# Kernel tuning notes

Measured on AMD Instinct MI355X. Metric: run time of the kernel, lower is better.

The kernel has to match this reference:

```python
import jax, jax.numpy as jnp
import numpy as np

SEQ = 4096
HIDDEN = 4096
HEAD_DIM = 1024
NUM_HEAD = HIDDEN // HEAD_DIM  # 4


def setup_inputs() -> dict:
    key = jax.random.key(0)
    ks = jax.random.split(key, 7)
    scale = 1.0 / np.sqrt(HIDDEN)  # torch Linear default-ish init scale
    h = jax.random.normal(ks[0], (SEQ, HIDDEN), dtype=jnp.float32)
    Wq = jax.random.normal(ks[1], (NUM_HEAD, HIDDEN, HEAD_DIM), dtype=jnp.float32) * scale
    bq = jax.random.normal(ks[2], (NUM_HEAD, HEAD_DIM), dtype=jnp.float32) * scale
    Wk = jax.random.normal(ks[3], (NUM_HEAD, HIDDEN, HEAD_DIM), dtype=jnp.float32) * scale
    bk = jax.random.normal(ks[4], (NUM_HEAD, HEAD_DIM), dtype=jnp.float32) * scale
    Wv = jax.random.normal(ks[5], (NUM_HEAD, HIDDEN, HEAD_DIM), dtype=jnp.float32) * scale
    bv = jax.random.normal(ks[6], (NUM_HEAD, HEAD_DIM), dtype=jnp.float32) * scale
    return {"h": h, "Wq": Wq, "bq": bq, "Wk": Wk, "bk": bk, "Wv": Wv, "bv": bv}


def reference(h, Wq, bq, Wk, bk, Wv, bv):
    # Batched per-head projections: q/k/v [H, S, E]
    q = jnp.einsum('sd,hde->hse', h, Wq) + bq[:, None, :]
    k = jnp.einsum('sd,hde->hse', h, Wk) + bk[:, None, :]
    v = jnp.einsum('sd,hde->hse', h, Wv) + bv[:, None, :]
    # Full (non-causal) attention scores [H, S, S], scaled by sqrt(head_dim)
    s = jnp.einsum('hse,hte->hst', q, k) / jnp.sqrt(jnp.asarray(HEAD_DIM, h.dtype))
    p = jax.nn.softmax(s, axis=-1)
    out = jnp.einsum('hst,hte->hse', p, v)  # [H, S, E]
    # Concatenate heads along feature dim -> [S, H*E]
    return jnp.transpose(out, (1, 0, 2)).reshape(h.shape[0], -1)
```

## Files before the change

kernel.cpp:

```cpp
#include <hip/hip_runtime.h>

#define SEQ   4096
#define HID   4096
#define EDIM  1024
#define NHEAD 4

typedef __attribute__((ext_vector_type(8))) short short8;
typedef __attribute__((ext_vector_type(16))) float f32x16;

typedef const __attribute__((address_space(1))) void* gas_ptr;
typedef __attribute__((address_space(3))) void* las_ptr;
#define GLD16(g, l) __builtin_amdgcn_global_load_lds((gas_ptr)(g), (las_ptr)(l), 16, 0, 0)

#define BARRIER() __builtin_amdgcn_s_barrier()
#define SCHED0()  __builtin_amdgcn_sched_barrier(0)
#define LGKM0()   asm volatile("s_waitcnt lgkmcnt(0)" ::: "memory")
#define VMC(N)    asm volatile("s_waitcnt vmcnt(" #N ")" ::: "memory")

__device__ __forceinline__ unsigned short f2bf(float f) {
  union { float f; unsigned u; } v; v.f = f;
  unsigned r = v.u + 0x7fffu + ((v.u >> 16) & 1u);
  return (unsigned short)(r >> 16);
}
__device__ __forceinline__ float bf2f(unsigned short u) {
  union { unsigned u; float f; } v; v.u = ((unsigned)u) << 16;
  return v.f;
}

__global__ __launch_bounds__(256) void hconv_kernel(const float* __restrict__ in,
                                                    unsigned short* __restrict__ out) {
  size_t i = ((size_t)blockIdx.x * 256 + threadIdx.x) * 8;
  const float4 a = *(const float4*)(in + i);
  const float4 b = *(const float4*)(in + i + 4);
  short8 o;
  o[0] = (short)f2bf(a.x); o[1] = (short)f2bf(a.y);
  o[2] = (short)f2bf(a.z); o[3] = (short)f2bf(a.w);
  o[4] = (short)f2bf(b.x); o[5] = (short)f2bf(b.y);
  o[6] = (short)f2bf(b.z); o[7] = (short)f2bf(b.w);
  *(short8*)(out + i) = o;
}

__global__ __launch_bounds__(256) void wconv_kernel(const float* __restrict__ Wq,
                                                    const float* __restrict__ Wk,
                                                    const float* __restrict__ Wv,
                                                    unsigned short* __restrict__ wt) {
  const int mh = blockIdx.y;
  const int mat = mh >> 2, head = mh & 3;
  const float* W = (mat == 0 ? Wq : (mat == 1 ? Wk : Wv)) + (size_t)head * HID * EDIM;
  unsigned short* out = wt + (size_t)mh * EDIM * HID;
  const int tile = blockIdx.x;
  const int td = tile >> 4;
  const int te = tile & 15;
  __shared__ float lds[64][65];
  const int tid = threadIdx.x;
  const int r = tid >> 4, c4 = (tid & 15) * 4;
#pragma unroll
  for (int it = 0; it < 4; ++it) {
    int dr = r + 16 * it;
    const float4 v = *(const float4*)&W[(size_t)(td * 64 + dr) * EDIM + te * 64 + c4];
    lds[dr][c4 + 0] = v.x; lds[dr][c4 + 1] = v.y;
    lds[dr][c4 + 2] = v.z; lds[dr][c4 + 3] = v.w;
  }
  __syncthreads();
#pragma unroll
  for (int it = 0; it < 4; ++it) {
    int er = r + 16 * it;
    ushort4 o;
    o.x = f2bf(lds[c4 + 0][er]); o.y = f2bf(lds[c4 + 1][er]);
    o.z = f2bf(lds[c4 + 2][er]); o.w = f2bf(lds[c4 + 3][er]);
    *(ushort4*)&out[(size_t)(te * 64 + er) * HID + td * 64 + c4] = o;
  }
}

template <int MODE>
__global__ __launch_bounds__(512, 2) void gemm256_kernel(
    const unsigned short* __restrict__ Aall, const unsigned short* __restrict__ Ball,
    long long aBatch, long long bBatch, int K,
    const float* __restrict__ biasAll, long long biasBatch,
    void* __restrict__ outAll, long long outBatch, int ldOut, float scale,
    int gx, int gxy) {
  extern __shared__ char smem[];

  const int nwg = (int)gridDim.x;
  const int lin = (int)blockIdx.x;
  int wg = (lin & 7) * (nwg >> 3) + (lin >> 3);
  const int z = wg / gxy; wg -= z * gxy;
  const int by = wg / gx;
  const int bx = wg - by * gx;
  const int bm = by * 256, bn = bx * 256;

  const unsigned short* A = Aall + (size_t)z * aBatch;
  const unsigned short* B = Ball + (size_t)z * bBatch;

  const int tid = threadIdx.x;
  const int lane = tid & 63, wid = tid >> 6;
  const int wr = wid >> 2, wc = wid & 3;
  const int la31 = lane & 31, lg2 = lane >> 5;

  const int srow = tid >> 3;
  const int sk = ((tid & 7) ^ ((srow ^ (srow >> 3)) & 7)) * 8;
  const unsigned short* aS00 = A + (size_t)(bm +   0 + srow) * K + sk;
  const unsigned short* aS01 = A + (size_t)(bm +  64 + srow) * K + sk;
  const unsigned short* aS10 = A + (size_t)(bm + 128 + srow) * K + sk;
  const unsigned short* aS11 = A + (size_t)(bm + 192 + srow) * K + sk;
  const unsigned short* bS00 = B + (size_t)(bn +   0 + srow) * K + sk;
  const unsigned short* bS01 = B + (size_t)(bn +  64 + srow) * K + sk;
  const unsigned short* bS10 = B + (size_t)(bn + 128 + srow) * K + sk;
  const unsigned short* bS11 = B + (size_t)(bn + 192 + srow) * K + sk;

#define STG(p0, p1, regionOff, tt)                                        \
  do {                                                                    \
    char* _d = smem + (((tt) & 1) << 16) + (regionOff) + tid * 16;        \
    GLD16((p0) + (size_t)(tt) * 64, _d);                                  \
    GLD16((p1) + (size_t)(tt) * 64, _d + 8192);                           \
  } while (0)

  int aO[4], aX[4];
#pragma unroll
  for (int m = 0; m < 4; ++m) {
    const int arow = wr * 128 + m * 32 + la31;
    aO[m] = arow * 128;
    aX[m] = (arow ^ (arow >> 3)) & 7;
  }
  int bO[2], bX[2];
#pragma unroll
  for (int n = 0; n < 2; ++n) {
    const int brow = wc * 64 + n * 32 + la31;
    bO[n] = 32768 + brow * 128;
    bX[n] = (brow ^ (brow >> 3)) & 7;
  }

  f32x16 acc[4][2];
#pragma unroll
  for (int m = 0; m < 4; ++m)
#pragma unroll
    for (int n = 0; n < 2; ++n)
#pragma unroll
      for (int r = 0; r < 16; ++r) acc[m][n][r] = 0.f;

  const int NT = K >> 6;

  STG(aS00, aS01, 0, 0);
  STG(aS10, aS11, 16384, 0);
  STG(bS00, bS01, 32768, 0);
  STG(bS10, bS11, 49152, 0);

  short8 av[2][4], bv[2][4];

  for (int t = 0; t < NT; ++t) {
    const char* base = smem + ((t & 1) << 16);

    VMC(0);
    BARRIER();
    SCHED0();

#pragma unroll
    for (int m = 0; m < 2; ++m)
#pragma unroll
      for (int ks = 0; ks < 4; ++ks)
        av[m][ks] = *(const short8*)(base + aO[m] + ((((ks << 1) + lg2) ^ aX[m]) << 4));
#pragma unroll
    for (int n = 0; n < 2; ++n)
#pragma unroll
      for (int ks = 0; ks < 4; ++ks)
        bv[n][ks] = *(const short8*)(base + bO[n] + ((((ks << 1) + lg2) ^ bX[n]) << 4));
    if (t + 1 < NT) {
      STG(aS00, aS01, 0, t + 1);
      STG(aS10, aS11, 16384, t + 1);
      STG(bS00, bS01, 32768, t + 1);
      STG(bS10, bS11, 49152, t + 1);
    }
    LGKM0();
    SCHED0();
    __builtin_amdgcn_s_setprio(1);
#pragma unroll
    for (int ks = 0; ks < 4; ++ks)
#pragma unroll
      for (int m = 0; m < 2; ++m)
#pragma unroll
        for (int n = 0; n < 2; ++n)
          acc[m][n] = __builtin_amdgcn_mfma_f32_32x32x16_bf16(av[m][ks], bv[n][ks], acc[m][n], 0, 0, 0);
    __builtin_amdgcn_s_setprio(0);

#pragma unroll
    for (int m = 0; m < 2; ++m)
#pragma unroll
      for (int ks = 0; ks < 4; ++ks)
        av[m][ks] = *(const short8*)(base + aO[m + 2] + ((((ks << 1) + lg2) ^ aX[m + 2]) << 4));
    LGKM0();
    SCHED0();
    __builtin_amdgcn_s_setprio(1);
#pragma unroll
    for (int ks = 0; ks < 4; ++ks)
#pragma unroll
      for (int m = 0; m < 2; ++m)
#pragma unroll
        for (int n = 0; n < 2; ++n)
          acc[m + 2][n] = __builtin_amdgcn_mfma_f32_32x32x16_bf16(av[m][ks], bv[n][ks], acc[m + 2][n], 0, 0, 0);
    __builtin_amdgcn_s_setprio(0);
    SCHED0();
  }
#undef STG

  float bvv[2];
  if (MODE == 0 || MODE == 1) {
    const float* bias = biasAll + (size_t)z * biasBatch;
#pragma unroll
    for (int n = 0; n < 2; ++n) bvv[n] = bias[bn + wc * 64 + n * 32 + la31];
  }
#pragma unroll
  for (int m = 0; m < 4; ++m)
#pragma unroll
    for (int n = 0; n < 2; ++n)
#pragma unroll
      for (int r = 0; r < 16; ++r) {
        const int grow = bm + wr * 128 + m * 32 + (r & 3) + 8 * (r >> 2) + 4 * lg2;
        const int gcol = bn + wc * 64 + n * 32 + la31;
        float val = acc[m][n][r];
        if (MODE == 0 || MODE == 1) val += bvv[n];
        if (MODE == 2) val *= scale;
        if (MODE == 0 || MODE == 2) {
          unsigned short* o = (unsigned short*)outAll + (size_t)z * outBatch;
          o[(size_t)grow * ldOut + gcol] = f2bf(val);
        } else if (MODE == 1) {
          unsigned short* o = (unsigned short*)outAll + (size_t)z * outBatch;
          o[(size_t)gcol * ldOut + grow] = f2bf(val);
        } else {
          float* o = (float*)outAll + (size_t)z * outBatch;
          o[(size_t)grow * ldOut + gcol] = val;
        }
      }
}

__global__ __launch_bounds__(256) void softmax_kernel(unsigned short* __restrict__ Sb) {
  const size_t row = blockIdx.x;
  unsigned short* p = Sb + row * (size_t)SEQ;
  const int tid = threadIdx.x;
  const int lane = tid & 63, wid = tid >> 6;
  float v[16];
  const short8 u0 = *(const short8*)&p[tid * 16];
  const short8 u1 = *(const short8*)&p[tid * 16 + 8];
#pragma unroll
  for (int j = 0; j < 8; ++j) v[j] = bf2f((unsigned short)u0[j]);
#pragma unroll
  for (int j = 0; j < 8; ++j) v[8 + j] = bf2f((unsigned short)u1[j]);
  float mx = v[0];
#pragma unroll
  for (int j = 1; j < 16; ++j) mx = fmaxf(mx, v[j]);
#pragma unroll
  for (int off = 32; off; off >>= 1) mx = fmaxf(mx, __shfl_xor(mx, off));
  __shared__ float red[8];
  if (lane == 0) red[wid] = mx;
  __syncthreads();
  mx = fmaxf(fmaxf(red[0], red[1]), fmaxf(red[2], red[3]));
  float s = 0.f;
#pragma unroll
  for (int j = 0; j < 16; ++j) { v[j] = __expf(v[j] - mx); s += v[j]; }
#pragma unroll
  for (int off = 32; off; off >>= 1) s += __shfl_xor(s, off);
  if (lane == 0) red[4 + wid] = s;
  __syncthreads();
  s = (red[4] + red[5]) + (red[6] + red[7]);
  const float inv = 1.0f / s;
  short8 o0, o1;
#pragma unroll
  for (int j = 0; j < 8; ++j) o0[j] = (short)f2bf(v[j] * inv);
#pragma unroll
  for (int j = 0; j < 8; ++j) o1[j] = (short)f2bf(v[8 + j] * inv);
  *(short8*)&p[tid * 16] = o0;
  *(short8*)&p[tid * 16 + 8] = o1;
}

extern "C" void kernel_launch(void* const* d_in, const int* in_sizes, int n_in,
                              void* d_out, int out_size, void* d_ws, size_t ws_size,
                              hipStream_t stream) {
  const float* h  = (const float*)d_in[0];
  const float* Wq = (const float*)d_in[1];
  const float* bq = (const float*)d_in[2];
  const float* Wk = (const float*)d_in[3];
  const float* bk = (const float*)d_in[4];
  const float* Wv = (const float*)d_in[5];
  const float* bv = (const float*)d_in[6];
  float* out = (float*)d_out;
  char* ws = (char*)d_ws;

  (void)hipFuncSetAttribute((const void*)&gemm256_kernel<0>,
                            hipFuncAttributeMaxDynamicSharedMemorySize, 131072);
  (void)hipFuncSetAttribute((const void*)&gemm256_kernel<1>,
                            hipFuncAttributeMaxDynamicSharedMemorySize, 131072);
  (void)hipFuncSetAttribute((const void*)&gemm256_kernel<2>,
                            hipFuncAttributeMaxDynamicSharedMemorySize, 131072);
  (void)hipFuncSetAttribute((const void*)&gemm256_kernel<3>,
                            hipFuncAttributeMaxDynamicSharedMemorySize, 131072);

  unsigned short* hB = (unsigned short*)ws;
  unsigned short* wt = (unsigned short*)(ws + (32ull << 20));
  unsigned short* Sb = (unsigned short*)ws;
  unsigned short* Qb = (unsigned short*)(ws + (128ull << 20));
  unsigned short* Kb = (unsigned short*)(ws + (160ull << 20));
  unsigned short* Vt = (unsigned short*)(ws + (192ull << 20));

  const long long WED = (long long)EDIM * HID;
  const long long QKB = (long long)SEQ * EDIM;
  const long long SSB = (long long)SEQ * SEQ;

  hconv_kernel<<<dim3((SEQ * (size_t)HID) / (256 * 8)), 256, 0, stream>>>(h, hB);
  wconv_kernel<<<dim3((HID / 64) * (EDIM / 64), 12), 256, 0, stream>>>(Wq, Wk, Wv, wt);

  gemm256_kernel<0><<<dim3(4 * 16 * 4), 512, 131072, stream>>>(
      hB, wt + 0 * WED, 0, WED, HID, bq, EDIM, Qb, QKB, EDIM, 1.f, 4, 64);
  gemm256_kernel<0><<<dim3(4 * 16 * 4), 512, 131072, stream>>>(
      hB, wt + 4 * WED, 0, WED, HID, bk, EDIM, Kb, QKB, EDIM, 1.f, 4, 64);
  gemm256_kernel<1><<<dim3(4 * 16 * 4), 512, 131072, stream>>>(
      hB, wt + 8 * WED, 0, WED, HID, bv, EDIM, Vt, QKB, SEQ, 1.f, 4, 64);

  gemm256_kernel<2><<<dim3(16 * 16 * 4), 512, 131072, stream>>>(
      Qb, Kb, QKB, QKB, EDIM, nullptr, 0, Sb, SSB, SEQ, 0.03125f, 16, 256);

  softmax_kernel<<<dim3(NHEAD * SEQ), 256, 0, stream>>>(Sb);

  gemm256_kernel<3><<<dim3(4 * 16 * 4), 512, 131072, stream>>>(
      Sb, Vt, SSB, QKB, SEQ, nullptr, 0, out, (long long)EDIM, NHEAD * EDIM, 1.f, 4, 64);
}
```

Baseline: 797.4 us.

## Software-pipeline GEMM main loop with register double-buffered LDS fragments

Reworks the bf16 GEMM inner loop so each 64-wide k-tile is processed as four k-slices. The LDS fragment reads for the next slice are issued into a second register set while MFMAs run on the current one, and the first slice of the next tile is prefetched after the barrier. The explicit lgkmcnt waits are dropped, and a second barrier per iteration protects the LDS buffer before it is overwritten. The aim is to hide LDS read latency behind matrix-core work, at the cost of an extra barrier per k-tile and more scheduling pressure on the compiler.

```diff
diff --git a/kernel.cpp b/kernel.cpp
--- a/kernel.cpp
+++ b/kernel.cpp
@@ -14,8 +14,7 @@
 
 #define BARRIER() __builtin_amdgcn_s_barrier()
 #define SCHED0()  __builtin_amdgcn_sched_barrier(0)
-#define LGKM0()   asm volatile("s_waitcnt lgkmcnt(0)" ::: "memory")
-#define VMC(N)    asm volatile("s_waitcnt vmcnt(" #N ")" ::: "memory")
+#define VMC0()    asm volatile("s_waitcnt vmcnt(0)" ::: "memory")
 
 __device__ __forceinline__ unsigned short f2bf(float f) {
   union { float f; unsigned u; } v; v.f = f;
@@ -99,20 +98,26 @@
 
   const int srow = tid >> 3;
   const int sk = ((tid & 7) ^ ((srow ^ (srow >> 3)) & 7)) * 8;
-  const unsigned short* aS00 = A + (size_t)(bm +   0 + srow) * K + sk;
-  const unsigned short* aS01 = A + (size_t)(bm +  64 + srow) * K + sk;
-  const unsigned short* aS10 = A + (size_t)(bm + 128 + srow) * K + sk;
-  const unsigned short* aS11 = A + (size_t)(bm + 192 + srow) * K + sk;
-  const unsigned short* bS00 = B + (size_t)(bn +   0 + srow) * K + sk;
-  const unsigned short* bS01 = B + (size_t)(bn +  64 + srow) * K + sk;
-  const unsigned short* bS10 = B + (size_t)(bn + 128 + srow) * K + sk;
-  const unsigned short* bS11 = B + (size_t)(bn + 192 + srow) * K + sk;
-
-#define STG(p0, p1, regionOff, tt)                                        \
+  const unsigned short* aS0 = A + (size_t)(bm +   0 + srow) * K + sk;
+  const unsigned short* aS1 = A + (size_t)(bm +  64 + srow) * K + sk;
+  const unsigned short* aS2 = A + (size_t)(bm + 128 + srow) * K + sk;
+  const unsigned short* aS3 = A + (size_t)(bm + 192 + srow) * K + sk;
+  const unsigned short* bS0 = B + (size_t)(bn +   0 + srow) * K + sk;
+  const unsigned short* bS1 = B + (size_t)(bn +  64 + srow) * K + sk;
+  const unsigned short* bS2 = B + (size_t)(bn + 128 + srow) * K + sk;
+  const unsigned short* bS3 = B + (size_t)(bn + 192 + srow) * K + sk;
+
+#define STG(tt)                                                           \
   do {                                                                    \
-    char* _d = smem + (((tt) & 1) << 16) + (regionOff) + tid * 16;        \
-    GLD16((p0) + (size_t)(tt) * 64, _d);                                  \
-    GLD16((p1) + (size_t)(tt) * 64, _d + 8192);                           \
+    char* _d = smem + (((tt) & 1) << 16) + tid * 16;                      \
+    GLD16(aS0 + (size_t)(tt) * 64, _d);                                   \
+    GLD16(aS1 + (size_t)(tt) * 64, _d + 8192);                            \
+    GLD16(aS2 + (size_t)(tt) * 64, _d + 16384);                          \
+    GLD16(aS3 + (size_t)(tt) * 64, _d + 24576);                          \
+    GLD16(bS0 + (size_t)(tt) * 64, _d + 32768);                          \
+    GLD16(bS1 + (size_t)(tt) * 64, _d + 40960);                          \
+    GLD16(bS2 + (size_t)(tt) * 64, _d + 49152);                          \
+    GLD16(bS3 + (size_t)(tt) * 64, _d + 57344);                          \
   } while (0)
 
   int aO[4], aX[4];
@@ -130,6 +135,22 @@
     bX[n] = (brow ^ (brow >> 3)) & 7;
   }
 
+#define RD_A(SET, BASE, KS)                                               \
+  _Pragma("unroll") for (int m = 0; m < 4; ++m)                           \
+    SET[m] = *(const short8*)((BASE) + aO[m] +                            \
+                              (((((KS) << 1) + lg2) ^ aX[m]) << 4));
+#define RD_B(SET, BASE, KS)                                               \
+  _Pragma("unroll") for (int n = 0; n < 2; ++n)                           \
+    SET[n] = *(const short8*)((BASE) + bO[n] +                            \
+                              (((((KS) << 1) + lg2) ^ bX[n]) << 4));
+#define MFMA_S(AV, BV)                                                    \
+  __builtin_amdgcn_s_setprio(1);                                          \
+  _Pragma("unroll") for (int m = 0; m < 4; ++m)                           \
+  _Pragma("unroll") for (int n = 0; n < 2; ++n)                           \
+    acc[m][n] = __builtin_amdgcn_mfma_f32_32x32x16_bf16(                  \
+        AV[m], BV[n], acc[m][n], 0, 0, 0);                                \
+  __builtin_amdgcn_s_setprio(0);
+
   f32x16 acc[4][2];
 #pragma unroll
   for (int m = 0; m < 4; ++m)
@@ -140,67 +161,46 @@
 
   const int NT = K >> 6;
 
-  STG(aS00, aS01, 0, 0);
-  STG(aS10, aS11, 16384, 0);
-  STG(bS00, bS01, 32768, 0);
-  STG(bS10, bS11, 49152, 0);
-
-  short8 av[2][4], bv[2][4];
+  short8 avA[4], bvA[2], avB[4], bvB[2];
+
+  STG(0);
+  VMC0();
+  BARRIER();
+  RD_A(avA, smem, 0); RD_B(bvA, smem, 0);
+  SCHED0();
 
   for (int t = 0; t < NT; ++t) {
-    const char* base = smem + ((t & 1) << 16);
-
-    VMC(0);
+    const char* base  = smem + ((t & 1) << 16);
+    const char* nbase = smem + (((t + 1) & 1) << 16);
+
+    if (t + 1 < NT) STG(t + 1);
+    RD_A(avB, base, 1); RD_B(bvB, base, 1);
+    SCHED0();
+    MFMA_S(avA, bvA);
+    SCHED0();
+
+    RD_A(avA, base, 2); RD_B(bvA, base, 2);
+    SCHED0();
+    MFMA_S(avB, bvB);
+    SCHED0();
+
+    RD_A(avB, base, 3); RD_B(bvB, base, 3);
+    SCHED0();
+    MFMA_S(avA, bvA);
+    SCHED0();
+
+    VMC0();
     BARRIER();
-    SCHED0();
-
-#pragma unroll
-    for (int m = 0; m < 2; ++m)
-#pragma unroll
-      for (int ks = 0; ks < 4; ++ks)
-        av[m][ks] = *(const short8*)(base + aO[m] + ((((ks << 1) + lg2) ^ aX[m]) << 4));
-#pragma unroll
-    for (int n = 0; n < 2; ++n)
-#pragma unroll
-      for (int ks = 0; ks < 4; ++ks)
-        bv[n][ks] = *(const short8*)(base + bO[n] + ((((ks << 1) + lg2) ^ bX[n]) << 4));
-    if (t + 1 < NT) {
-      STG(aS00, aS01, 0, t + 1);
-      STG(aS10, aS11, 16384, t + 1);
-      STG(bS00, bS01, 32768, t + 1);
-      STG(bS10, bS11, 49152, t + 1);
-    }
-    LGKM0();
-    SCHED0();
-    __builtin_amdgcn_s_setprio(1);
-#pragma unroll
-    for (int ks = 0; ks < 4; ++ks)
-#pragma unroll
-      for (int m = 0; m < 2; ++m)
-#pragma unroll
-        for (int n = 0; n < 2; ++n)
-          acc[m][n] = __builtin_amdgcn_mfma_f32_32x32x16_bf16(av[m][ks], bv[n][ks], acc[m][n], 0, 0, 0);
-    __builtin_amdgcn_s_setprio(0);
-
-#pragma unroll
-    for (int m = 0; m < 2; ++m)
-#pragma unroll
-      for (int ks = 0; ks < 4; ++ks)
-        av[m][ks] = *(const short8*)(base + aO[m + 2] + ((((ks << 1) + lg2) ^ aX[m + 2]) << 4));
-    LGKM0();
-    SCHED0();
-    __builtin_amdgcn_s_setprio(1);
-#pragma unroll
-    for (int ks = 0; ks < 4; ++ks)
-#pragma unroll
-      for (int m = 0; m < 2; ++m)
-#pragma unroll
-        for (int n = 0; n < 2; ++n)
-          acc[m + 2][n] = __builtin_amdgcn_mfma_f32_32x32x16_bf16(av[m][ks], bv[n][ks], acc[m + 2][n], 0, 0, 0);
-    __builtin_amdgcn_s_setprio(0);
-    SCHED0();
+    if (t + 1 < NT) { RD_A(avA, nbase, 0); RD_B(bvA, nbase, 0); }
+    SCHED0();
+    MFMA_S(avB, bvB);
+    SCHED0();
+    BARRIER();
   }
 #undef STG
+#undef RD_A
+#undef RD_B
+#undef MFMA_S
 
   float bvv[2];
   if (MODE == 0 || MODE == 1) {
```

Result: no change. 783.3 us (-1.8%).
